# Performance work log

Measured on AMD Instinct MI355X. Metric: run time of the kernel, lower is better.

Reference implementation:

```python
import numpy as np
import jax
import jax.numpy as jnp
from collections import deque

NUM_CLASSES = 32
N_PARENTS = 4
N_CHILD = 7
SINK_WEIGHT = 0.1
EPS = 1e-7
B, D, H, W = 2, 96, 96, 96

# ---- static tree construction (mirrors adjacency_matrix / bitpack_tree / reachability) ----

def _build_adjacency():
    n = NUM_CLASSES + 1  # node 0 is the virtual root
    A = np.zeros((n, n), dtype=np.int64)
    for p in range(N_PARENTS):
        A[0, 1 + p] = 1
        for c in range(N_CHILD):
            A[1 + p, 1 + N_PARENTS + p * N_CHILD + c] = 1
    return A

ADJ = _build_adjacency()

def _reachability(A):
    # R[i, j] = 1 iff j is reachable from i (i is ancestor-or-self of j)
    R = np.eye(A.shape[0], dtype=bool) | (A > 0)
    for _ in range(A.shape[0]):
        Rn = R | (R @ (A > 0))
        if (Rn == R).all():
            break
        R = Rn
    return R

def _bitpack(A):
    # each node's bitmask encodes its path from the root; (x & group) == class tests descendant-ness
    n = A.shape[0]
    bc = np.zeros(n, dtype=np.int64)
    bg = np.zeros(n, dtype=np.int64)
    bit = 0
    q = deque([0])
    while q:
        p = q.popleft()
        ch = np.nonzero(A[p])[0]
        if len(ch) == 0:
            continue
        w = int(np.ceil(np.log2(len(ch) + 1)))
        for i, c in enumerate(ch):
            bc[c] = bc[p] | ((i + 1) << bit)
            bg[c] = bg[p] | (((1 << w) - 1) << bit)
            q.append(c)
        bit += w
    return bc, bg

_BC, _BG = _bitpack(ADJ)
BM_CLASS = _BC[1:].astype(np.int32)
BM_GROUP = _BG[1:].astype(np.int32)
RMT = _reachability(ADJ)[1:, 1:].T.astype(np.float32)  # RMT[label, c] = c is ancestor-or-self
LEAF = np.nonzero(ADJ[1:, 1:].sum(axis=1) == 0)[0].astype(np.int32)
_SIB = ((ADJ.T @ ADJ) > 0)[1:, 1:]
SINK_IDS = [N_PARENTS + p * N_CHILD for p in range(N_PARENTS)]
PARENT_OF = {s: int(ADJ[1:, 1:][:, s].argmax()) for s in SINK_IDS}
SIBS = {}
for _s in SINK_IDS:
    _row = _SIB[_s].copy()
    _row[_s] = False
    SIBS[_s] = np.nonzero(_row)[0].tolist()
# DDESC[l, c] = 1 iff class l is a descendant-or-self of class c (bitmask test)
DDESC = ((BM_CLASS[:, None] & BM_GROUP[None, :]) == BM_CLASS[None, :]).astype(np.float32)


def setup_inputs() -> dict:
    key = jax.random.key(0)
    k1, k2 = jax.random.split(key)
    images = jax.random.normal(k1, (B, NUM_CLASSES, D, H, W), dtype=jnp.float32)
    targets = jax.random.randint(k2, (B, D, H, W), 0, NUM_CLASSES, dtype=jnp.int32)
    masks = jnp.ones((B, NUM_CLASSES), dtype=bool)
    return {"images": images, "targets": targets, "masks": masks}


def reference(images, targets, masks):
    C = NUM_CLASSES
    probs = jax.nn.softmax(images, axis=1)  # activation_fn over class dim
    leaf = jnp.asarray(LEAF)
    pred = leaf[jnp.argmax(probs[:, LEAF], axis=1)]  # _argmax_leaves -> [B,D,H,W] int32
    bm_class = jnp.asarray(BM_CLASS)
    rmt = jnp.asarray(RMT)
    ddesc = jnp.asarray(DDESC)

    def per_sample(p, pr, y, m):
        p = p.reshape(C, -1).T          # [N, C] probabilities
        y = y.reshape(-1)
        pr = pr.reshape(-1)
        valid = y != 255
        vw = valid.astype(p.dtype)
        y_safe = jnp.where(valid, y, 0).astype(jnp.int32)
        mf = m.astype(p.dtype)

        # ---- sink dice (hierarchical sink/sibling logic) ----
        pred_bm = bm_class[pr]
        sds, fls = [], []
        for s in SINK_IDS:
            sib_mask = jnp.zeros_like(valid)
            for sib in SIBS[s]:
                sib_mask = sib_mask | (y_safe == sib) | ((~m[sib]) & (pr == sib))
            par = PARENT_OF[s]
            pmask = (pred_bm & int(BM_GROUP[par])) == int(BM_CLASS[par])
            tgt = (pmask & (~sib_mask)).astype(p.dtype) * vw
            pp = p[:, s] * vw
            inter = jnp.sum(pp * tgt)
            d = 1.0 - (2.0 * inter + 1e-5) / (jnp.sum(pp) + jnp.sum(tgt) + 1e-5)
            sds.append(d)
            fls.append((jnp.sum(sib_mask & valid) > 0).astype(p.dtype))
        sd = jnp.stack(sds)
        fl = jnp.stack(fls)
        cnt = fl.sum()
        sink_dice = SINK_WEIGHT * jnp.where(cnt > 0, jnp.sum(sd * fl) / jnp.maximum(cnt, 1.0), 0.0)

        # ---- main dice (smooth_nr=0) + hierarchical CE over masked classes ----
        t = rmt[y_safe]                 # [N, C] multi-hot (label + ancestors)
        wcol = vw[:, None]
        inter = jnp.sum(p * t * wcol, axis=0)
        denom = jnp.sum(p * wcol, axis=0) + jnp.sum(t * wcol, axis=0)
        dice_c = 1.0 - (2.0 * inter) / (denom + 1e-5)
        dice = jnp.sum(dice_c * mf) / jnp.maximum(mf.sum(), 1.0)

        logp = jnp.log(jnp.clip(p, EPS, 1.0 - EPS))
        ce = jnp.sum(-jnp.sum(t * logp * mf[None, :], axis=1) * vw) / jnp.maximum(vw.sum(), 1.0)

        # ---- confusion matrix via joint (pred, true) histogram + descendant matrix ----
        flat = pr.astype(jnp.int32) * C + y_safe
        hist = jnp.zeros((C * C,), p.dtype).at[flat].add(vw).reshape(C, C)  # [pred, true]
        tp = jnp.einsum('lc,lt,tc->c', ddesc, hist, ddesc)
        fp = jnp.einsum('lc,lt->c', ddesc, hist) - tp
        fn = jnp.einsum('lt,tc->c', hist, ddesc) - tp
        cm = jnp.stack([tp, fp, fn], axis=-1) * mf[:, None]
        return jnp.stack([ce, dice, sink_dice]), cm

    loss, cm = jax.vmap(per_sample)(probs, pred, targets, masks)
    return loss, cm, pred
```

## Files before the change

### kernel.cpp

```cpp
#include <hip/hip_runtime.h>

#define NC 32
#define NVOX (96*96*96)
#define NB 512
#define TPB 256

#define WS_CE     0
#define WS_SP     32
#define WS_SPT    64
#define WS_SINKI  96
#define WS_SIB    100
#define WS_TGT    104
#define WS_HIST   128
#define SLOT_STRIDE 1152
#define NSLOT     (2 * NB)
#define FINAL_OFF (NSLOT * SLOT_STRIDE)
#define CTR_IDX   124
#define NCHUNK    8
#define BLK_PER_CH (NB / NCHUNK)
#define RED_BLK_X ((2 * SLOT_STRIDE + TPB - 1) / TPB)
#define RED_NBLK  (RED_BLK_X * NCHUNK)

__device__ __forceinline__ float wave_reduce(float v) {
    #pragma unroll
    for (int off = 32; off > 0; off >>= 1)
        v += __shfl_down(v, off, 64);
    return v;
}

__global__ __launch_bounds__(TPB, 4) void voxel_kernel(
    const float* __restrict__ images,
    const int*   __restrict__ targets,
    const int*   __restrict__ masks,
    float* __restrict__ ws,
    float* __restrict__ pred_out)
{
    const int slot = blockIdx.x;
    const int b    = slot & 1;
    const int blk  = slot >> 1;
    const int tid  = threadIdx.x;

    __shared__ float s_hist[NC * NC];
    __shared__ float s_spt[NC];
    __shared__ float s_mf[NC];
    __shared__ float s_red[45];

    for (int i = tid; i < NC * NC; i += TPB) s_hist[i] = 0.f;
    if (tid < 45) s_red[tid] = 0.f;
    if (tid < NC) {
        s_spt[tid] = 0.f;
        s_mf[tid]  = (masks[b * NC + tid] != 0) ? 1.f : 0.f;
    }
    if (slot == 0) {
        float* wsf = ws + FINAL_OFF;
        for (int i = tid; i < 2 * SLOT_STRIDE; i += TPB) wsf[i] = 0.f;
        if (tid == 0) *(unsigned int*)(ws + CTR_IDX) = 0u;
    }
    __syncthreads();

    const float* img  = images + (size_t)b * NC * NVOX;
    const int*   tgt  = targets + (size_t)b * NVOX;
    float*       pout = pred_out + (size_t)b * NVOX;
    float*       wsb  = ws + (size_t)slot * SLOT_STRIDE;

    float sp[NC];
    #pragma unroll
    for (int c = 0; c < NC; ++c) sp[c] = 0.f;
    float ce = 0.f;
    float sinkI[4] = {0.f, 0.f, 0.f, 0.f};
    float sibc[4]  = {0.f, 0.f, 0.f, 0.f};
    float tgtc[4]  = {0.f, 0.f, 0.f, 0.f};

    for (int v = blk * TPB + tid; v < NVOX; v += NB * TPB) {
        const int  y     = tgt[v];
        const bool valid = (y != 255);
        const int  ysafe = valid ? y : 0;
        const float vwf  = valid ? 1.f : 0.f;
        const int  py    = (ysafe >= 4) ? (ysafe - 4) / 7 : -1;
        const int  pyi   = (py >= 0) ? py : 0;

        float ev[NC];
        float sum = 0.f, best = -3.4e38f;
        float pyv_e = 0.f, ppv_e = 0.f, cur = 0.f, esk = 0.f;
        int   pred = 4;
        #pragma unroll
        for (int c = 0; c < NC; ++c) {
            const float x = img[(size_t)c * NVOX + v];
            const float e = __expf(x);
            ev[c] = e;
            sum  += e;
            pyv_e = (c == ysafe) ? e : pyv_e;
            if (c < 4)
                ppv_e = (c == pyi) ? e : ppv_e;
            if (c >= 4 && ((c - 4) % 7) == 0)
                cur = e;
            if (c >= 4) {
                const bool g = (x > best);
                best = g ? x : best;
                pred = g ? c : pred;
                esk  = g ? cur : esk;
            }
        }
        const float rinv = 1.f / sum;
        pout[v] = (float)pred;

        const int pp = (pred - 4) / 7;
        const float pyv  = pyv_e * rinv;
        const float ppv  = ppv_e * rinv;
        const float eskv = esk   * rinv;

        float term = __logf(fminf(fmaxf(pyv, 1e-7f), 1.f - 1e-7f)) * s_mf[ysafe];
        if (py >= 0)
            term += __logf(fminf(fmaxf(ppv, 1e-7f), 1.f - 1e-7f)) * s_mf[pyi];
        ce -= term * vwf;

        atomicAdd(&s_spt[ysafe], pyv * vwf);
        if (py >= 0) atomicAdd(&s_spt[pyi], ppv * vwf);

        atomicAdd(&s_hist[pred * NC + ysafe], vwf);

        const bool pm = (s_mf[pred] == 0.f);
        #pragma unroll
        for (int k = 0; k < 4; ++k) {
            const int  sk   = 4 + 7 * k;
            const bool ysib = (py == k) && (ysafe != sk);
            const bool msib = pm && (pp == k) && (pred != sk);
            const bool sib  = ysib || msib;
            if (sib && valid) sibc[k] += 1.f;
            if ((pp == k) && !sib && valid) {
                tgtc[k]  += 1.f;
                sinkI[k] += eskv;
            }
        }

        const float rw = rinv * vwf;
        #pragma unroll
        for (int c = 0; c < NC; ++c)
            sp[c] = __builtin_fmaf(ev[c], rw, sp[c]);
    }

    const int lane = tid & 63;
    {
        float r = wave_reduce(ce);
        if (lane == 0) atomicAdd(&s_red[0], r);
    }
    #pragma unroll
    for (int c = 0; c < NC; ++c) {
        float r = wave_reduce(sp[c]);
        if (lane == 0) atomicAdd(&s_red[1 + c], r);
    }
    #pragma unroll
    for (int k = 0; k < 4; ++k) {
        float r = wave_reduce(sinkI[k]);
        if (lane == 0) atomicAdd(&s_red[33 + k], r);
        r = wave_reduce(sibc[k]);
        if (lane == 0) atomicAdd(&s_red[37 + k], r);
        r = wave_reduce(tgtc[k]);
        if (lane == 0) atomicAdd(&s_red[41 + k], r);
    }
    __syncthreads();

    for (int i = tid; i < NC * NC; i += TPB) wsb[WS_HIST + i] = s_hist[i];
    if (tid == 0) wsb[WS_CE] = s_red[0];
    if (tid < NC) {
        wsb[WS_SP  + tid] = s_red[1 + tid];
        wsb[WS_SPT + tid] = s_spt[tid];
    }
    if (tid < 4) {
        wsb[WS_SINKI + tid] = s_red[33 + tid];
        wsb[WS_SIB   + tid] = s_red[37 + tid];
        wsb[WS_TGT   + tid] = s_red[41 + tid];
    }
}

__global__ __launch_bounds__(TPB) void reduce_kernel(
    const float* __restrict__ ws,
    float* __restrict__ wsf,
    const int* __restrict__ masks,
    float* __restrict__ out,
    unsigned int* __restrict__ ctr)
{
    const int v = blockIdx.x * TPB + threadIdx.x;
    {
        const int b    = v / SLOT_STRIDE;
        const int val  = v % SLOT_STRIDE;
        const int blk0 = blockIdx.y * BLK_PER_CH;
        const float* base = ws + (size_t)b * SLOT_STRIDE + val;
        float s = 0.f;
        #pragma unroll 8
        for (int i = 0; i < BLK_PER_CH; ++i)
            s += base[(size_t)(2 * (blk0 + i)) * SLOT_STRIDE];
        atomicAdd(&wsf[v], s);
    }

    __shared__ unsigned int s_last;
    __threadfence();
    __syncthreads();
    if (threadIdx.x == 0) s_last = atomicAdd(ctr, 1u);
    __syncthreads();
    if (s_last != RED_NBLK - 1) return;
    __threadfence();

    __shared__ float f_col[2][NC], f_row[2][NC], f_dice[2][NC], f_mf[2][NC];
    const int t  = threadIdx.x & 63;
    const int fb = threadIdx.x >> 6;
    const bool act = (fb < 2) && (t < NC);

    if (act) {
        const float* hist = wsf + (size_t)fb * SLOT_STRIDE + WS_HIST;
        float cs = 0.f, rs = 0.f;
        for (int j = 0; j < NC; ++j) {
            cs += hist[j * NC + t];
            rs += hist[t * NC + j];
        }
        f_col[fb][t] = cs;
        f_row[fb][t] = rs;
        f_mf[fb][t]  = (masks[fb * NC + t] != 0) ? 1.f : 0.f;
    }
    __syncthreads();

    if (act) {
        const float* wsb  = wsf + (size_t)fb * SLOT_STRIDE;
        const float* hist = wsb + WS_HIST;
        const int c = t;
        float ycnt, pcnt, tp;
        if (c < 4) {
            int idx[8];
            idx[0] = c;
            for (int j = 0; j < 7; ++j) idx[1 + j] = 4 + 7 * c + j;
            ycnt = f_col[fb][c]; pcnt = f_row[fb][c];
            for (int j = 0; j < 7; ++j) { ycnt += f_col[fb][idx[1 + j]]; pcnt += f_row[fb][idx[1 + j]]; }
            tp = 0.f;
            for (int a = 0; a < 8; ++a)
                for (int d = 0; d < 8; ++d)
                    tp += hist[idx[a] * NC + idx[d]];
        } else {
            ycnt = f_col[fb][c]; pcnt = f_row[fb][c];
            tp = hist[c * NC + c];
        }
        const float mf = f_mf[fb][c];
        out[6 + (fb * NC + c) * 3 + 0] = tp * mf;
        out[6 + (fb * NC + c) * 3 + 1] = (pcnt - tp) * mf;
        out[6 + (fb * NC + c) * 3 + 2] = (ycnt - tp) * mf;
        f_dice[fb][c] = (1.f - 2.f * wsb[WS_SPT + c] / (wsb[WS_SP + c] + ycnt + 1e-5f)) * mf;
    }
    __syncthreads();

    if (fb < 2 && t == 0) {
        const float* wsb = wsf + (size_t)fb * SLOT_STRIDE;
        float vw = 0.f, dsum = 0.f, msum = 0.f;
        for (int c = 0; c < NC; ++c) {
            vw   += f_col[fb][c];
            dsum += f_dice[fb][c];
            msum += f_mf[fb][c];
        }
        const float cel  = wsb[WS_CE] / fmaxf(vw, 1.f);
        const float dice = dsum / fmaxf(msum, 1.f);
        float cnt = 0.f, sd = 0.f;
        for (int k = 0; k < 4; ++k) {
            float fl = (wsb[WS_SIB + k] > 0.f) ? 1.f : 0.f;
            float d  = 1.f - (2.f * wsb[WS_SINKI + k] + 1e-5f) /
                             (wsb[WS_SP + 4 + 7 * k] + wsb[WS_TGT + k] + 1e-5f);
            cnt += fl;
            sd  += d * fl;
        }
        out[fb * 3 + 0] = cel;
        out[fb * 3 + 1] = dice;
        out[fb * 3 + 2] = (cnt > 0.f) ? 0.1f * (sd / fmaxf(cnt, 1.f)) : 0.f;
    }
}

extern "C" void kernel_launch(void* const* d_in, const int* in_sizes, int n_in,
                              void* d_out, int out_size, void* d_ws, size_t ws_size,
                              hipStream_t stream) {
    const float* images  = (const float*)d_in[0];
    const int*   targets = (const int*)d_in[1];
    const int*   masks   = (const int*)d_in[2];
    float* out = (float*)d_out;
    float* ws  = (float*)d_ws;
    float* wsf = ws + FINAL_OFF;

    voxel_kernel<<<dim3(NSLOT), dim3(TPB), 0, stream>>>(
        images, targets, masks, ws, out + 6 + 2 * NC * 3);
    reduce_kernel<<<dim3(RED_BLK_X, NCHUNK), dim3(TPB), 0, stream>>>(
        ws, wsf, masks, out, (unsigned int*)(ws + CTR_IDX));
}
```

Baseline: 344.0 us.

## Process two voxels per thread with float2/int2 vectorized loads

Each thread now handles a pair of adjacent voxels, loading logits, targets and writing predictions as float2/int2 to widen memory transactions. Grid size drops from 512 to 384 blocks per sample and launch bounds go to 3 waves per SIMD, leaving room for the doubled register arrays. The sink-probability selection moves from an in-loop tracker to a post-loop select among four class values. The cost is higher register pressure (two 32-element exp arrays), which may cause spilling or lower occupancy.

```diff
diff --git a/kernel.cpp b/kernel.cpp
--- a/kernel.cpp
+++ b/kernel.cpp
@@ -2,7 +2,8 @@
 
 #define NC 32
 #define NVOX (96*96*96)
-#define NB 512
+#define NPAIR (NVOX/2)
+#define NB 384
 #define TPB 256
 
 #define WS_CE     0
@@ -28,7 +29,7 @@
     return v;
 }
 
-__global__ __launch_bounds__(TPB, 4) void voxel_kernel(
+__global__ __launch_bounds__(TPB, 3) void voxel_kernel(
     const float* __restrict__ images,
     const int*   __restrict__ targets,
     const int*   __restrict__ masks,
@@ -58,10 +59,10 @@
     }
     __syncthreads();
 
-    const float* img  = images + (size_t)b * NC * NVOX;
-    const int*   tgt  = targets + (size_t)b * NVOX;
-    float*       pout = pred_out + (size_t)b * NVOX;
-    float*       wsb  = ws + (size_t)slot * SLOT_STRIDE;
+    const float2* img2 = (const float2*)(images + (size_t)b * NC * NVOX);
+    const int2*   tgt2 = (const int2*)(targets + (size_t)b * NVOX);
+    float2*       pout2 = (float2*)(pred_out + (size_t)b * NVOX);
+    float*        wsb  = ws + (size_t)slot * SLOT_STRIDE;
 
     float sp[NC];
     #pragma unroll
@@ -71,72 +72,105 @@
     float sibc[4]  = {0.f, 0.f, 0.f, 0.f};
     float tgtc[4]  = {0.f, 0.f, 0.f, 0.f};
 
-    for (int v = blk * TPB + tid; v < NVOX; v += NB * TPB) {
-        const int  y     = tgt[v];
-        const bool valid = (y != 255);
-        const int  ysafe = valid ? y : 0;
-        const float vwf  = valid ? 1.f : 0.f;
-        const int  py    = (ysafe >= 4) ? (ysafe - 4) / 7 : -1;
-        const int  pyi   = (py >= 0) ? py : 0;
-
-        float ev[NC];
-        float sum = 0.f, best = -3.4e38f;
-        float pyv_e = 0.f, ppv_e = 0.f, cur = 0.f, esk = 0.f;
-        int   pred = 4;
+    for (int vp = blk * TPB + tid; vp < NPAIR; vp += NB * TPB) {
+        const int2 y2 = tgt2[vp];
+
+        const bool validA = (y2.x != 255);
+        const bool validB = (y2.y != 255);
+        const int  ysA = validA ? y2.x : 0;
+        const int  ysB = validB ? y2.y : 0;
+        const float vwA = validA ? 1.f : 0.f;
+        const float vwB = validB ? 1.f : 0.f;
+        const int  pyA = (ysA >= 4) ? (ysA - 4) / 7 : -1;
+        const int  pyB = (ysB >= 4) ? (ysB - 4) / 7 : -1;
+        const int  pyiA = (pyA >= 0) ? pyA : 0;
+        const int  pyiB = (pyB >= 0) ? pyB : 0;
+
+        float eva[NC], evb[NC];
+        float sumA = 0.f, sumB = 0.f;
+        float bestA = -3.4e38f, bestB = -3.4e38f;
+        float pyvA = 0.f, pyvB = 0.f, ppvA = 0.f, ppvB = 0.f;
+        int   predA = 4, predB = 4;
         #pragma unroll
         for (int c = 0; c < NC; ++c) {
-            const float x = img[(size_t)c * NVOX + v];
-            const float e = __expf(x);
-            ev[c] = e;
-            sum  += e;
-            pyv_e = (c == ysafe) ? e : pyv_e;
-            if (c < 4)
-                ppv_e = (c == pyi) ? e : ppv_e;
-            if (c >= 4 && ((c - 4) % 7) == 0)
-                cur = e;
+            const float2 x2 = img2[(size_t)c * NPAIR + vp];
+            const float ea = __expf(x2.x);
+            const float eb = __expf(x2.y);
+            eva[c] = ea;  evb[c] = eb;
+            sumA += ea;   sumB += eb;
+            pyvA = (c == ysA) ? ea : pyvA;
+            pyvB = (c == ysB) ? eb : pyvB;
+            if (c < 4) {
+                ppvA = (c == pyiA) ? ea : ppvA;
+                ppvB = (c == pyiB) ? eb : ppvB;
+            }
             if (c >= 4) {
-                const bool g = (x > best);
-                best = g ? x : best;
-                pred = g ? c : pred;
-                esk  = g ? cur : esk;
+                const bool gA = (x2.x > bestA);
+                bestA = gA ? x2.x : bestA;
+                predA = gA ? c : predA;
+                const bool gB = (x2.y > bestB);
+                bestB = gB ? x2.y : bestB;
+                predB = gB ? c : predB;
             }
         }
-        const float rinv = 1.f / sum;
-        pout[v] = (float)pred;
-
-        const int pp = (pred - 4) / 7;
-        const float pyv  = pyv_e * rinv;
-        const float ppv  = ppv_e * rinv;
-        const float eskv = esk   * rinv;
-
-        float term = __logf(fminf(fmaxf(pyv, 1e-7f), 1.f - 1e-7f)) * s_mf[ysafe];
-        if (py >= 0)
-            term += __logf(fminf(fmaxf(ppv, 1e-7f), 1.f - 1e-7f)) * s_mf[pyi];
-        ce -= term * vwf;
-
-        atomicAdd(&s_spt[ysafe], pyv * vwf);
-        if (py >= 0) atomicAdd(&s_spt[pyi], ppv * vwf);
-
-        atomicAdd(&s_hist[pred * NC + ysafe], vwf);
-
-        const bool pm = (s_mf[pred] == 0.f);
+        const float rinvA = 1.f / sumA;
+        const float rinvB = 1.f / sumB;
+        float2 pw; pw.x = (float)predA; pw.y = (float)predB;
+        pout2[vp] = pw;
+
+        const int ppA = (predA - 4) / 7;
+        const int ppB = (predB - 4) / 7;
+        const float eskA = (ppA == 0) ? eva[4] : (ppA == 1) ? eva[11]
+                         : (ppA == 2) ? eva[18] : eva[25];
+        const float eskB = (ppB == 0) ? evb[4] : (ppB == 1) ? evb[11]
+                         : (ppB == 2) ? evb[18] : evb[25];
+
+        const float pA  = pyvA * rinvA, pB  = pyvB * rinvB;
+        const float qA  = ppvA * rinvA, qB  = ppvB * rinvB;
+        const float skA = eskA * rinvA, skB = eskB * rinvB;
+
+        float termA = __logf(fminf(fmaxf(pA, 1e-7f), 1.f - 1e-7f)) * s_mf[ysA];
+        if (pyA >= 0)
+            termA += __logf(fminf(fmaxf(qA, 1e-7f), 1.f - 1e-7f)) * s_mf[pyiA];
+        float termB = __logf(fminf(fmaxf(pB, 1e-7f), 1.f - 1e-7f)) * s_mf[ysB];
+        if (pyB >= 0)
+            termB += __logf(fminf(fmaxf(qB, 1e-7f), 1.f - 1e-7f)) * s_mf[pyiB];
+        ce -= termA * vwA + termB * vwB;
+
+        atomicAdd(&s_spt[ysA], pA * vwA);
+        if (pyA >= 0) atomicAdd(&s_spt[pyiA], qA * vwA);
+        atomicAdd(&s_spt[ysB], pB * vwB);
+        if (pyB >= 0) atomicAdd(&s_spt[pyiB], qB * vwB);
+
+        atomicAdd(&s_hist[predA * NC + ysA], vwA);
+        atomicAdd(&s_hist[predB * NC + ysB], vwB);
+
+        const bool pmA = (s_mf[predA] == 0.f);
+        const bool pmB = (s_mf[predB] == 0.f);
         #pragma unroll
         for (int k = 0; k < 4; ++k) {
-            const int  sk   = 4 + 7 * k;
-            const bool ysib = (py == k) && (ysafe != sk);
-            const bool msib = pm && (pp == k) && (pred != sk);
-            const bool sib  = ysib || msib;
-            if (sib && valid) sibc[k] += 1.f;
-            if ((pp == k) && !sib && valid) {
-                tgtc[k]  += 1.f;
-                sinkI[k] += eskv;
+            const int sk = 4 + 7 * k;
+            {
+                const bool ysib = (pyA == k) && (ysA != sk);
+                const bool msib = pmA && (ppA == k) && (predA != sk);
+                const bool sib  = ysib || msib;
+                if (sib && validA) sibc[k] += 1.f;
+                if ((ppA == k) && !sib && validA) { tgtc[k] += 1.f; sinkI[k] += skA; }
             }
-        }
-
-        const float rw = rinv * vwf;
+            {
+                const bool ysib = (pyB == k) && (ysB != sk);
+                const bool msib = pmB && (ppB == k) && (predB != sk);
+                const bool sib  = ysib || msib;
+                if (sib && validB) sibc[k] += 1.f;
+                if ((ppB == k) && !sib && validB) { tgtc[k] += 1.f; sinkI[k] += skB; }
+            }
+        }
+
+        const float rwA = rinvA * vwA;
+        const float rwB = rinvB * vwB;
         #pragma unroll
         for (int c = 0; c < NC; ++c)
-            sp[c] = __builtin_fmaf(ev[c], rw, sp[c]);
+            sp[c] = __builtin_fmaf(evb[c], rwB, __builtin_fmaf(eva[c], rwA, sp[c]));
     }
 
     const int lane = tid & 63;
```

Result: no change. 345.2 us (+0.3%).
